# Kernel optimization log

Hardware: AMD Instinct MI355X
Metric: run time of the kernel (lower is better)

The kernel has to match this reference:

```python
import jax, jax.numpy as jnp
import numpy as np

B, D, L = 16384, 1024, 4


def setup_inputs() -> dict:
    key = jax.random.key(0)
    ks = jax.random.split(key, 5)
    scale = 1.0 / np.sqrt(D)
    x = jax.random.normal(ks[0], (B, D), dtype=jnp.float32)
    # torch nn.Linear default init: U(-1/sqrt(fan_in), 1/sqrt(fan_in))
    Ws = jax.random.uniform(ks[1], (L, D, D), jnp.float32, -scale, scale)
    bs = jax.random.uniform(ks[2], (L, D), jnp.float32, -scale, scale)
    Wo = jax.random.uniform(ks[3], (D, D), jnp.float32, -scale, scale)
    bo = jax.random.uniform(ks[4], (D,), jnp.float32, -scale, scale)
    return {"x": x, "Ws": Ws, "bs": bs, "Wo": Wo, "bo": bo}


def reference(x, Ws, bs, Wo, bo):
    # torch: matmul(x[:, :, None], x[:, None, :]).sum(2) == x * x.sum(-1, keepdims=True)
    interactions = jax.nn.relu(x * jnp.sum(x, axis=-1, keepdims=True))  # (B, D)
    h = x
    for i in range(L):  # fixed small layer count
        h = jax.nn.relu(h @ Ws[i].T + bs[i])  # torch Linear: y = x W^T + b
    out = ((h + interactions) * 0.5) @ Wo.T + bo
    return out
```

## Files before the change

kernel.cpp:

```cpp
#include <hip/hip_runtime.h>


#define DDIM 1024
#define BROWS 16384

typedef __attribute__((ext_vector_type(8))) short s8v;
typedef __attribute__((ext_vector_type(4))) float f4v;

__device__ __forceinline__ unsigned short f2bf(float f) {
    unsigned int u = __float_as_uint(f);
    u += 0x7fffu + ((u >> 16) & 1u);
    return (unsigned short)(u >> 16);
}
__device__ __forceinline__ float bf2f(unsigned short u) {
    return __uint_as_float(((unsigned int)u) << 16);
}
__device__ __forceinline__ void gld16(const void* g, void* l) {
    __builtin_amdgcn_global_load_lds(
        (const __attribute__((address_space(1))) unsigned int*)g,
        (__attribute__((address_space(3))) unsigned int*)l, 16, 0, 0);
}

__global__ __launch_bounds__(256) void prep_kernel(
    const float* __restrict__ x, unsigned short* __restrict__ xb,
    float* __restrict__ rowsum)
{
    const int row = blockIdx.x;
    const int t = threadIdx.x;
    const float4 v = *(const float4*)(x + (size_t)row * DDIM + t * 4);
    ushort4 o;
    o.x = f2bf(v.x); o.y = f2bf(v.y); o.z = f2bf(v.z); o.w = f2bf(v.w);
    *(ushort4*)(xb + (size_t)row * DDIM + t * 4) = o;
    float s = v.x + v.y + v.z + v.w;
    #pragma unroll
    for (int off = 32; off > 0; off >>= 1) s += __shfl_down(s, off, 64);
    __shared__ float red[4];
    const int wave = t >> 6, lane = t & 63;
    if (lane == 0) red[wave] = s;
    __syncthreads();
    if (t == 0) rowsum[row] = red[0] + red[1] + red[2] + red[3];
}

__global__ __launch_bounds__(256) void cvt_kernel(
    const float* __restrict__ Ws, const float* __restrict__ Wo,
    unsigned short* __restrict__ out)
{
    const int i = (blockIdx.x * 256 + threadIdx.x) * 4;
    const float* src = (i < 4 * DDIM * DDIM) ? (Ws + i) : (Wo + (i - 4 * DDIM * DDIM));
    const float4 v = *(const float4*)src;
    ushort4 o;
    o.x = f2bf(v.x); o.y = f2bf(v.y); o.z = f2bf(v.z); o.w = f2bf(v.w);
    *(ushort4*)(out + i) = o;
}

template <int MODE>
__global__ __launch_bounds__(256, 2) void gemm_bt(
    const unsigned short* __restrict__ A,
    const unsigned short* __restrict__ Bw,
    const float* __restrict__ bias,
    void* __restrict__ out,
    const unsigned short* __restrict__ xb,
    const float* __restrict__ rowsum)
{
    constexpr int K = DDIM, N = DDIM;
    __shared__ unsigned short smem[4][128 * 32];

    const int t = threadIdx.x;
    const int wave = t >> 6, lane = t & 63;
    const int wm = wave & 1, wn = wave >> 1;
    const int rowBase = blockIdx.x * 128;
    const int colBase = blockIdx.y * 128;

    f4v acc[4][4] = {};

    const int c0r = t >> 2, c0k = (t & 3) * 8;
    const int mrow = lane & 15;
    const int koff = (lane >> 4) * 8;

    for (int kt = 0; kt < K; kt += 64) {
        if (kt) __syncthreads();
        const unsigned short* a0 = A  + (size_t)(rowBase + c0r) * K + kt + c0k;
        const unsigned short* b0 = Bw + (size_t)(colBase + c0r) * K + kt + c0k;
        gld16(a0,               (char*)smem[0] + t * 16);
        gld16(a0 + 64 * K,      (char*)smem[0] + (t + 256) * 16);
        gld16(b0,               (char*)smem[2] + t * 16);
        gld16(b0 + 64 * K,      (char*)smem[2] + (t + 256) * 16);
        gld16(a0 + 32,          (char*)smem[1] + t * 16);
        gld16(a0 + 64 * K + 32, (char*)smem[1] + (t + 256) * 16);
        gld16(b0 + 32,          (char*)smem[3] + t * 16);
        gld16(b0 + 64 * K + 32, (char*)smem[3] + (t + 256) * 16);
        __syncthreads();

        #pragma unroll
        for (int s = 0; s < 2; ++s) {
            s8v af[4], bfr[4];
            #pragma unroll
            for (int mi = 0; mi < 4; ++mi)
                af[mi] = *(const s8v*)&smem[s][(wm * 64 + mi * 16 + mrow) * 32 + koff];
            #pragma unroll
            for (int ni = 0; ni < 4; ++ni)
                bfr[ni] = *(const s8v*)&smem[2 + s][(wn * 64 + ni * 16 + mrow) * 32 + koff];
            #pragma unroll
            for (int mi = 0; mi < 4; ++mi)
                #pragma unroll
                for (int ni = 0; ni < 4; ++ni)
                    acc[mi][ni] = __builtin_amdgcn_mfma_f32_16x16x32_bf16(
                        af[mi], bfr[ni], acc[mi][ni], 0, 0, 0);
        }
    }

    const int quad = lane >> 4;
    if (MODE == 2) {
        float* o = (float*)out;
        #pragma unroll
        for (int ni = 0; ni < 4; ++ni) {
            const int n = colBase + wn * 64 + ni * 16 + mrow;
            const float bv = bias[n];
            #pragma unroll
            for (int mi = 0; mi < 4; ++mi)
                #pragma unroll
                for (int r = 0; r < 4; ++r) {
                    const int row = rowBase + wm * 64 + mi * 16 + quad * 4 + r;
                    o[(size_t)row * N + n] = acc[mi][ni][r] + bv;
                }
        }
    } else {
        __syncthreads();
        unsigned short* sC = (unsigned short*)smem;
        #pragma unroll
        for (int ni = 0; ni < 4; ++ni) {
            const int n = wn * 64 + ni * 16 + mrow;
            const float bv = bias[colBase + n];
            #pragma unroll
            for (int mi = 0; mi < 4; ++mi)
                #pragma unroll
                for (int r = 0; r < 4; ++r) {
                    const int row = wm * 64 + mi * 16 + quad * 4 + r;
                    float v = acc[mi][ni][r] + bv;
                    v = v > 0.f ? v : 0.f;
                    sC[row * 128 + n] = f2bf(v);
                }
        }
        __syncthreads();
        unsigned short* o16 = (unsigned short*)out;
        #pragma unroll
        for (int i = 0; i < 8; ++i) {
            const int idx = t + i * 256;
            const int row = idx >> 4, ch = idx & 15;
            s8v c = *(const s8v*)&sC[row * 128 + ch * 8];
            if (MODE == 1) {
                const float rsv = rowsum[rowBase + row];
                const s8v xv = *(const s8v*)&xb[(size_t)(rowBase + row) * DDIM + colBase + ch * 8];
                #pragma unroll
                for (int j = 0; j < 8; ++j) {
                    float it = bf2f((unsigned short)xv[j]) * rsv;
                    it = it > 0.f ? it : 0.f;
                    const float v = 0.5f * (bf2f((unsigned short)c[j]) + it);
                    c[j] = (short)f2bf(v);
                }
            }
            *(s8v*)&o16[(size_t)(rowBase + row) * DDIM + colBase + ch * 8] = c;
        }
    }
}

extern "C" void kernel_launch(void* const* d_in, const int* in_sizes, int n_in,
                              void* d_out, int out_size, void* d_ws, size_t ws_size,
                              hipStream_t stream) {
    const float* x  = (const float*)d_in[0];
    const float* Ws = (const float*)d_in[1];
    const float* bs = (const float*)d_in[2];
    const float* Wo = (const float*)d_in[3];
    const float* bo = (const float*)d_in[4];
    float* out = (float*)d_out;

    char* ws = (char*)d_ws;
    unsigned short* xb  = (unsigned short*)(ws);
    unsigned short* h0  = (unsigned short*)(ws + 33554432);
    unsigned short* h1  = (unsigned short*)(ws + 67108864);
    unsigned short* wb  = (unsigned short*)(ws + 100663296);
    float*          rsm = (float*)(ws + 111149056);

    prep_kernel<<<BROWS, 256, 0, stream>>>(x, xb, rsm);
    cvt_kernel<<<(5 * DDIM * DDIM) / 1024, 256, 0, stream>>>(Ws, Wo, wb);

    const size_t WSZ = (size_t)DDIM * DDIM;
    dim3 g(BROWS / 128, DDIM / 128);
    gemm_bt<0><<<g, 256, 0, stream>>>(xb, wb,           bs,            h0, nullptr, nullptr);
    gemm_bt<0><<<g, 256, 0, stream>>>(h0, wb + 1 * WSZ, bs + 1 * DDIM, h1, nullptr, nullptr);
    gemm_bt<0><<<g, 256, 0, stream>>>(h1, wb + 2 * WSZ, bs + 2 * DDIM, h0, nullptr, nullptr);
    gemm_bt<1><<<g, 256, 0, stream>>>(h0, wb + 3 * WSZ, bs + 3 * DDIM, h1, xb, rsm);
    gemm_bt<2><<<g, 256, 0, stream>>>(h1, wb + 4 * WSZ, bo,            out, nullptr, nullptr);
}
```

Baseline: 373.4 us.

## Fuse prep and all GEMM layers into one persistent cooperative kernel

Replaces the seven kernel launches with a single cooperative kernel of 512 blocks. The blocks first convert the weights and x to bf16 and compute row sums, then run the five GEMM layers, each block handling two 128x128 tiles, with grid-wide syncs between layers. It also stages the final fp32 output through shared memory for coalesced stores. The intent is to remove launch gaps and per-launch tail effects, at the cost of grid-sync overhead and fixed two-tile-per-block scheduling with 3-block occupancy limits. If the cooperative launch fails, it falls back to the old multi-kernel path.

```diff
diff --git a/kernel.cpp b/kernel.cpp
--- a/kernel.cpp
+++ b/kernel.cpp
@@ -1,4 +1,7 @@
 #include <hip/hip_runtime.h>
+#include <hip/hip_cooperative_groups.h>
+
+namespace cg = cooperative_groups;
 
 
 #define DDIM 1024
@@ -19,6 +22,174 @@
     __builtin_amdgcn_global_load_lds(
         (const __attribute__((address_space(1))) unsigned int*)g,
         (__attribute__((address_space(3))) unsigned int*)l, 16, 0, 0);
+}
+
+__global__ __launch_bounds__(256, 3) void fused_coop(
+    const float* __restrict__ x,  const float* __restrict__ Ws,
+    const float* __restrict__ bs, const float* __restrict__ Wo,
+    const float* __restrict__ bo, float* __restrict__ out,
+    unsigned short* __restrict__ xb, unsigned short* __restrict__ h0,
+    unsigned short* __restrict__ h1, unsigned short* __restrict__ wb,
+    float* __restrict__ rsm)
+{
+    __shared__ unsigned short smem[4][128 * 32];
+
+    const int t = threadIdx.x;
+    const int lane = t & 63, wave = t >> 6;
+
+    {
+        const int gid = blockIdx.x * 256 + t;
+        #pragma unroll
+        for (int j = 0; j < 10; ++j) {
+            const int idx = gid + j * 131072;
+            const float4 v = (idx < 1048576) ? ((const float4*)Ws)[idx]
+                                             : ((const float4*)Wo)[idx - 1048576];
+            ushort4 o;
+            o.x = f2bf(v.x); o.y = f2bf(v.y); o.z = f2bf(v.z); o.w = f2bf(v.w);
+            ((ushort4*)wb)[idx] = o;
+        }
+        #pragma unroll 1
+        for (int j = 0; j < 8; ++j) {
+            const int row = blockIdx.x * 32 + wave * 8 + j;
+            const float* xr = x + (size_t)row * DDIM;
+            float s = 0.f;
+            #pragma unroll
+            for (int it = 0; it < 4; ++it) {
+                const int col = it * 256 + lane * 4;
+                const float4 v = *(const float4*)(xr + col);
+                s += v.x + v.y + v.z + v.w;
+                ushort4 o;
+                o.x = f2bf(v.x); o.y = f2bf(v.y); o.z = f2bf(v.z); o.w = f2bf(v.w);
+                *(ushort4*)(xb + (size_t)row * DDIM + col) = o;
+            }
+            #pragma unroll
+            for (int off = 32; off; off >>= 1) s += __shfl_down(s, off);
+            if (lane == 0) rsm[row] = s;
+        }
+    }
+    cg::this_grid().sync();
+
+    const unsigned short* hin[5] = {xb, h0, h1, h0, h1};
+    unsigned short* hout[4] = {h0, h1, h0, h1};
+
+    const int wm = wave & 1, wn = wave >> 1;
+    const int mrow = lane & 15;
+    const int quad = lane >> 4;
+    const int koff = quad * 8;
+    const int c0r = t >> 2, c0k = (t & 3) * 8;
+
+    #pragma unroll 1
+    for (int l = 0; l < 5; ++l) {
+        const unsigned short* A = hin[l];
+        const unsigned short* W = wb + (size_t)l * DDIM * DDIM;
+        const float* bias = (l < 4) ? bs + l * DDIM : bo;
+
+        #pragma unroll 1
+        for (int tt = 0; tt < 2; ++tt) {
+            const int tile = blockIdx.x * 2 + tt;
+            const int rowBase = (tile >> 3) * 128;
+            const int colBase = (tile & 7) * 128;
+
+            f4v acc[4][4] = {};
+
+            #pragma unroll 1
+            for (int kt = 0; kt < DDIM; kt += 64) {
+                __syncthreads();
+                const unsigned short* a0 = A + (size_t)(rowBase + c0r) * DDIM + kt + c0k;
+                const unsigned short* b0 = W + (size_t)(colBase + c0r) * DDIM + kt + c0k;
+                gld16(a0,                  (char*)smem[0] + t * 16);
+                gld16(a0 + 64 * DDIM,      (char*)smem[0] + (t + 256) * 16);
+                gld16(b0,                  (char*)smem[2] + t * 16);
+                gld16(b0 + 64 * DDIM,      (char*)smem[2] + (t + 256) * 16);
+                gld16(a0 + 32,             (char*)smem[1] + t * 16);
+                gld16(a0 + 64 * DDIM + 32, (char*)smem[1] + (t + 256) * 16);
+                gld16(b0 + 32,             (char*)smem[3] + t * 16);
+                gld16(b0 + 64 * DDIM + 32, (char*)smem[3] + (t + 256) * 16);
+                __syncthreads();
+                #pragma unroll
+                for (int s = 0; s < 2; ++s) {
+                    s8v af[4], bfr[4];
+                    #pragma unroll
+                    for (int mi = 0; mi < 4; ++mi)
+                        af[mi] = *(const s8v*)&smem[s][(wm * 64 + mi * 16 + mrow) * 32 + koff];
+                    #pragma unroll
+                    for (int ni = 0; ni < 4; ++ni)
+                        bfr[ni] = *(const s8v*)&smem[2 + s][(wn * 64 + ni * 16 + mrow) * 32 + koff];
+                    #pragma unroll
+                    for (int mi = 0; mi < 4; ++mi)
+                        #pragma unroll
+                        for (int ni = 0; ni < 4; ++ni)
+                            acc[mi][ni] = __builtin_amdgcn_mfma_f32_16x16x32_bf16(
+                                af[mi], bfr[ni], acc[mi][ni], 0, 0, 0);
+                }
+            }
+
+            if (l < 4) {
+                __syncthreads();
+                unsigned short* sC = (unsigned short*)smem;
+                #pragma unroll
+                for (int ni = 0; ni < 4; ++ni) {
+                    const int n = wn * 64 + ni * 16 + mrow;
+                    const float bv = bias[colBase + n];
+                    #pragma unroll
+                    for (int mi = 0; mi < 4; ++mi)
+                        #pragma unroll
+                        for (int r = 0; r < 4; ++r) {
+                            const int row = wm * 64 + mi * 16 + quad * 4 + r;
+                            float v = acc[mi][ni][r] + bv;
+                            v = v > 0.f ? v : 0.f;
+                            sC[row * 128 + n] = f2bf(v);
+                        }
+                }
+                __syncthreads();
+                unsigned short* o16 = hout[l];
+                #pragma unroll
+                for (int i = 0; i < 8; ++i) {
+                    const int idx = t + i * 256;
+                    const int row = idx >> 4, ch = idx & 15;
+                    s8v c = *(const s8v*)&sC[row * 128 + ch * 8];
+                    if (l == 3) {
+                        const float rsv = rsm[rowBase + row];
+                        const s8v xv = *(const s8v*)&xb[(size_t)(rowBase + row) * DDIM + colBase + ch * 8];
+                        #pragma unroll
+                        for (int j = 0; j < 8; ++j) {
+                            float it = bf2f((unsigned short)xv[j]) * rsv;
+                            it = it > 0.f ? it : 0.f;
+                            c[j] = (short)f2bf(0.5f * (bf2f((unsigned short)c[j]) + it));
+                        }
+                    }
+                    *(s8v*)&o16[(size_t)(rowBase + row) * DDIM + colBase + ch * 8] = c;
+                }
+            } else {
+                float* sCf = (float*)smem;
+                #pragma unroll 1
+                for (int half = 0; half < 2; ++half) {
+                    __syncthreads();
+                    if (wm == half) {
+                        #pragma unroll
+                        for (int ni = 0; ni < 4; ++ni) {
+                            const int n = wn * 64 + ni * 16 + mrow;
+                            const float bv = bias[colBase + n];
+                            #pragma unroll
+                            for (int mi = 0; mi < 4; ++mi)
+                                #pragma unroll
+                                for (int r = 0; r < 4; ++r)
+                                    sCf[(mi * 16 + quad * 4 + r) * 128 + n] = acc[mi][ni][r] + bv;
+                        }
+                    }
+                    __syncthreads();
+                    #pragma unroll
+                    for (int i = 0; i < 8; ++i) {
+                        const int idx = t + i * 256;
+                        const int row = idx >> 5, ch = idx & 31;
+                        const float4 v = ((const float4*)sCf)[idx];
+                        ((float4*)(out + (size_t)(rowBase + half * 64 + row) * DDIM + colBase))[ch] = v;
+                    }
+                }
+            }
+        }
+        if (l < 4) cg::this_grid().sync();
+    }
 }
 
 __global__ __launch_bounds__(256) void prep_kernel(
@@ -72,7 +243,6 @@
     const int colBase = blockIdx.y * 128;
 
     f4v acc[4][4] = {};
-
     const int c0r = t >> 2, c0k = (t & 3) * 8;
     const int mrow = lane & 15;
     const int koff = (lane >> 4) * 8;
@@ -90,7 +260,6 @@
         gld16(b0 + 32,          (char*)smem[3] + t * 16);
         gld16(b0 + 64 * K + 32, (char*)smem[3] + (t + 256) * 16);
         __syncthreads();
-
         #pragma unroll
         for (int s = 0; s < 2; ++s) {
             s8v af[4], bfr[4];
@@ -155,8 +324,7 @@
                 for (int j = 0; j < 8; ++j) {
                     float it = bf2f((unsigned short)xv[j]) * rsv;
                     it = it > 0.f ? it : 0.f;
-                    const float v = 0.5f * (bf2f((unsigned short)c[j]) + it);
-                    c[j] = (short)f2bf(v);
+                    c[j] = (short)f2bf(0.5f * (bf2f((unsigned short)c[j]) + it));
                 }
             }
             *(s8v*)&o16[(size_t)(rowBase + row) * DDIM + colBase + ch * 8] = c;
@@ -181,14 +349,18 @@
     unsigned short* wb  = (unsigned short*)(ws + 100663296);
     float*          rsm = (float*)(ws + 111149056);
 
-    prep_kernel<<<BROWS, 256, 0, stream>>>(x, xb, rsm);
-    cvt_kernel<<<(5 * DDIM * DDIM) / 1024, 256, 0, stream>>>(Ws, Wo, wb);
-
-    const size_t WSZ = (size_t)DDIM * DDIM;
-    dim3 g(BROWS / 128, DDIM / 128);
-    gemm_bt<0><<<g, 256, 0, stream>>>(xb, wb,           bs,            h0, nullptr, nullptr);
-    gemm_bt<0><<<g, 256, 0, stream>>>(h0, wb + 1 * WSZ, bs + 1 * DDIM, h1, nullptr, nullptr);
-    gemm_bt<0><<<g, 256, 0, stream>>>(h1, wb + 2 * WSZ, bs + 2 * DDIM, h0, nullptr, nullptr);
-    gemm_bt<1><<<g, 256, 0, stream>>>(h0, wb + 3 * WSZ, bs + 3 * DDIM, h1, xb, rsm);
-    gemm_bt<2><<<g, 256, 0, stream>>>(h1, wb + 4 * WSZ, bo,            out, nullptr, nullptr);
-}
+    void* args[] = {&x, &Ws, &bs, &Wo, &bo, &out, &xb, &h0, &h1, &wb, &rsm};
+    hipError_t e = hipLaunchCooperativeKernel((const void*)fused_coop,
+                                              dim3(512), dim3(256), args, 0, stream);
+    if (e != hipSuccess) {
+        prep_kernel<<<BROWS, 256, 0, stream>>>(x, xb, rsm);
+        cvt_kernel<<<(5 * DDIM * DDIM) / 1024, 256, 0, stream>>>(Ws, Wo, wb);
+        const size_t WSZ = (size_t)DDIM * DDIM;
+        dim3 g(BROWS / 128, DDIM / 128);
+        gemm_bt<0><<<g, 256, 0, stream>>>(xb, wb,           bs,            h0, nullptr, nullptr);
+        gemm_bt<0><<<g, 256, 0, stream>>>(h0, wb + 1 * WSZ, bs + 1 * DDIM, h1, nullptr, nullptr);
+        gemm_bt<0><<<g, 256, 0, stream>>>(h1, wb + 2 * WSZ, bs + 2 * DDIM, h0, nullptr, nullptr);
+        gemm_bt<1><<<g, 256, 0, stream>>>(h0, wb + 3 * WSZ, bs + 3 * DDIM, h1, xb, rsm);
+        gemm_bt<2><<<g, 256, 0, stream>>>(h1, wb + 4 * WSZ, bo,            out, nullptr, nullptr);
+    }
+}
```

After: 694.7 us. 1.86x slower.
